# Optimization experiments

Measured on AMD Instinct MI355X. Metric: run time of the kernel, lower is better.

## Reference

```python
import jax, jax.numpy as jnp
import numpy as np

K = 8  # knn_graph(k=8, loop=True): self-loop kept, so self is among the k nearest


def knn_idx(x, k):
    # x: [N, F]. Pairwise squared distances via the expansion trick.
    x2 = jnp.sum(x * x, axis=-1)                      # [N]
    d = x2[:, None] + x2[None, :] - 2.0 * (x @ x.T)   # [N, N]
    _, idx = jax.lax.top_k(-d, k)                     # [N, k] nearest (incl. self)
    return idx


def edge_conv(x, idx, W1, b1, W2, b2):
    # PyG EdgeConv: message = nn(cat([x_i, x_j - x_i])), aggr='max'.
    # Every node has exactly k incoming edges, so scatter-max == max over the k axis.
    n, f = x.shape
    k = idx.shape[1]
    xi = x[:, None, :]                                # [N, 1, F] center
    xj = x[idx]                                       # [N, k, F] neighbors (gather)
    e = jnp.concatenate([jnp.broadcast_to(xi, (n, k, f)), xj - xi], axis=-1)  # [N,k,2F]
    h = jax.nn.relu(e @ W1 + b1) @ W2 + b2            # [N, k, out]
    return jnp.max(h, axis=1)                         # [N, out]


def setup_inputs() -> dict:
    key = jax.random.key(0)
    ks = jax.random.split(key, 9)
    B, N, F = 2, 4096, 3
    H0, H1, OUT = 64, 128, 256

    def lin(kw, fan_in, fan_out):
        bound = 1.0 / np.sqrt(fan_in)
        kw1, kw2 = jax.random.split(kw)
        W = jax.random.uniform(kw1, (fan_in, fan_out), jnp.float32, -bound, bound)
        b = jax.random.uniform(kw2, (fan_out,), jnp.float32, -bound, bound)
        return W, b

    W1, b1 = lin(ks[0], 2 * F, H0)
    W2, b2 = lin(ks[1], H0, H1)
    W3, b3 = lin(ks[2], 2 * H1, H1)
    W4, b4 = lin(ks[3], H1, OUT)
    point_cloud = jax.random.normal(ks[4], (B, N, F), jnp.float32)
    return {"point_cloud": point_cloud, "W1": W1, "b1": b1, "W2": W2, "b2": b2,
            "W3": W3, "b3": b3, "W4": W4, "b4": b4}


def reference(point_cloud, W1, b1, W2, b2, W3, b3, W4, b4):
    B, N, F = point_cloud.shape
    pts = point_cloud.reshape(B * N, F)               # knn over ALL B*N points (no batch vec)
    idx = knn_idx(jax.lax.stop_gradient(pts), K)      # [B*N, K]
    x = jax.nn.relu(edge_conv(pts, idx, W1, b1, W2, b2))
    x = edge_conv(x, idx, W3, b3, W4, b4)
    return x.reshape(B, N, -1)
```

## Files before the change

kernel.cpp:

```cpp
#include <hip/hip_runtime.h>

#define NPTS 8192
#define NSLICE 64
#define SLICE_LEN (NPTS / NSLICE)
#define KNN 8
#define SURV_CAP 48

typedef short bf16x8 __attribute__((ext_vector_type(8)));
typedef float f32x4 __attribute__((ext_vector_type(4)));

__device__ __forceinline__ unsigned short f2bf(float x) {
  unsigned int u = __float_as_uint(x);
  return (unsigned short)((u + 0x7FFF + ((u >> 16) & 1)) >> 16);
}
__device__ __forceinline__ float bf2f(unsigned short s) {
  return __uint_as_float(((unsigned int)s) << 16);
}

__device__ __forceinline__ float dist_pk(float qx, float qy, float qz,
                                         float q2, float m2x, float m2y,
                                         float m2z, float p2) {
#pragma clang fp contract(off)
  float s = __fmaf_rn(qz, m2z, __fmaf_rn(qy, m2y, __fmaf_rn(qx, m2x, p2)));
  return __fadd_rn(q2, s);
}

__device__ __forceinline__ float norm2_exact(float x, float y, float z) {
#pragma clang fp contract(off)
  return __fadd_rn(__fadd_rn(__fmul_rn(x, x), __fmul_rn(y, y)),
                   __fmul_rn(z, z));
}

__device__ __forceinline__ float med3(float a, float b, float c) {
  return __builtin_amdgcn_fmed3f(a, b, c);
}

__device__ __forceinline__ double pack_key(float d, int idx) {
  unsigned int ub = __float_as_uint(d);
  ub ^= (((unsigned int)((int)ub >> 31)) | 0x80000000u);
  unsigned int lo = (ub << 13) | (unsigned int)idx;
  unsigned int hi = 0x3ff00000u | (ub >> 19);
  return __hiloint2double((int)hi, (int)lo);
}

#define KEY_DECL                                                            \
  const double KINF = __longlong_as_double(0x7ff0000000000000LL);           \
  double k0 = KINF, k1 = KINF, k2 = KINF, k3 = KINF, k4 = KINF, k5 = KINF,  \
         k6 = KINF, k7 = KINF;
#define KB1(s)                                                              \
  {                                                                         \
    double mn = fmin(carry, k##s);                                          \
    carry = fmax(carry, k##s);                                              \
    k##s = mn;                                                              \
  }
#define KEY_INSERT(key)                                                     \
  {                                                                         \
    double carry = (key);                                                   \
    KB1(0) KB1(1) KB1(2) KB1(3) KB1(4) KB1(5) KB1(6) KB1(7)                 \
  }

#define VINS(dv)                                                            \
  {                                                                         \
    float dd = (dv);                                                        \
    v7 = med3(dd, v6, v7);                                                  \
    v6 = med3(dd, v5, v6);                                                  \
    v5 = med3(dd, v4, v5);                                                  \
    v4 = med3(dd, v3, v4);                                                  \
    v3 = med3(dd, v2, v3);                                                  \
    v2 = med3(dd, v1, v2);                                                  \
    v1 = med3(dd, v0, v1);                                                  \
    v0 = fminf(dd, v0);                                                     \
  }

#define VDECL                                                               \
  const float FINF = __uint_as_float(0x7f800000u);                          \
  float v0 = FINF, v1 = FINF, v2 = FINF, v3 = FINF, v4 = FINF, v5 = FINF,   \
        v6 = FINF, v7 = FINF;

#define VINS2(dv)                                                           \
  {                                                                         \
    float dd = (dv);                                                        \
    s1 = med3(dd, s0, s1);                                                  \
    s0 = fminf(dd, s0);                                                     \
  }

__global__ __launch_bounds__(256) void knn_vals_kernel(
    const float* __restrict__ pts, float* __restrict__ part_v,
    float4* __restrict__ pts4) {
  __shared__ float4 sp[SLICE_LEN];
  const int t = threadIdx.x;
  const int q = blockIdx.x * 256 + t;
  const int jbase = blockIdx.y * SLICE_LEN;
  for (int p = t; p < SLICE_LEN; p += 256) {
    float x = pts[(jbase + p) * 3 + 0];
    float yy = pts[(jbase + p) * 3 + 1];
    float z = pts[(jbase + p) * 3 + 2];
    float4 v = make_float4(__fmul_rn(-2.0f, x), __fmul_rn(-2.0f, yy),
                           __fmul_rn(-2.0f, z), norm2_exact(x, yy, z));
    sp[p] = v;
    if (blockIdx.x == 0) pts4[jbase + p] = v;
  }
  __syncthreads();
  const float qx = pts[q * 3 + 0], qy = pts[q * 3 + 1], qz = pts[q * 3 + 2];
  const float q2 = norm2_exact(qx, qy, qz);
  const float FINF = __uint_as_float(0x7f800000u);
  float s0 = FINF, s1 = FINF;
  for (int p = 0; p < SLICE_LEN; p += 8) {
    float4 c0 = sp[p + 0];
    float4 c1 = sp[p + 1];
    float4 c2 = sp[p + 2];
    float4 c3 = sp[p + 3];
    float4 c4 = sp[p + 4];
    float4 c5 = sp[p + 5];
    float4 c6 = sp[p + 6];
    float4 c7 = sp[p + 7];
    float d0 = dist_pk(qx, qy, qz, q2, c0.x, c0.y, c0.z, c0.w);
    float d1 = dist_pk(qx, qy, qz, q2, c1.x, c1.y, c1.z, c1.w);
    float d2 = dist_pk(qx, qy, qz, q2, c2.x, c2.y, c2.z, c2.w);
    float d3 = dist_pk(qx, qy, qz, q2, c3.x, c3.y, c3.z, c3.w);
    float d4 = dist_pk(qx, qy, qz, q2, c4.x, c4.y, c4.z, c4.w);
    float d5 = dist_pk(qx, qy, qz, q2, c5.x, c5.y, c5.z, c5.w);
    float d6 = dist_pk(qx, qy, qz, q2, c6.x, c6.y, c6.z, c6.w);
    float d7 = dist_pk(qx, qy, qz, q2, c7.x, c7.y, c7.z, c7.w);
    VINS2(d0);
    VINS2(d1);
    VINS2(d2);
    VINS2(d3);
    VINS2(d4);
    VINS2(d5);
    VINS2(d6);
    VINS2(d7);
  }
  float* o = &part_v[(size_t)(blockIdx.y * 2) * NPTS + q];
  o[0 * NPTS] = s0;
  o[1 * NPTS] = s1;
}

__global__ __launch_bounds__(256) void knn_collect_kernel(
    const float4* __restrict__ pts4, const float* __restrict__ part_v,
    int* __restrict__ nbr, const float* __restrict__ W2,
    const float* __restrict__ W3, const float* __restrict__ W4,
    unsigned short* __restrict__ W2th, unsigned short* __restrict__ W2tl,
    unsigned short* __restrict__ W3th, unsigned short* __restrict__ W3tl,
    unsigned short* __restrict__ W4ht, unsigned short* __restrict__ W4lt) {
  __shared__ double keybuf[4][SURV_CAP];
  __shared__ int scnt[4];
  __shared__ float v8s[4][8][9];
  __shared__ float smin[4][65];
  __shared__ float thrS[4];
  __shared__ unsigned long long maskS[4];
  const int t = threadIdx.x;
  if (blockIdx.x < 128) {
    const int id = blockIdx.x * 256 + t;
    const int k = id >> 8, c = id & 255;
    {
      float v = W4[k * 256 + c];
      unsigned short hi = f2bf(v);
      W4ht[c * 128 + k] = hi;
      W4lt[c * 128 + k] = f2bf(v - bf2f(hi));
    }
    {
      float v3 = (c < 128) ? W3[k * 128 + c] : W3[(128 + k) * 128 + (c - 128)];
      unsigned short h3 = f2bf(v3);
      W3th[c * 128 + k] = h3;
      W3tl[c * 128 + k] = f2bf(v3 - bf2f(h3));
    }
    if (id < NPTS) {
      const int kk = id >> 7, cc = id & 127;
      float v2 = W2[kk * 128 + cc];
      unsigned short h2 = f2bf(v2);
      W2th[cc * 64 + kk] = h2;
      W2tl[cc * 64 + kk] = f2bf(v2 - bf2f(h2));
    }
  }
  const int wv = t >> 6;
  const int lane = t & 63;
  const int q = blockIdx.x * 4 + wv;
  if (lane == 0) scnt[wv] = 0;

  if (t < 32) {
    const int lq = t >> 3, c = t & 7;
    const int qq = blockIdx.x * 4 + lq;
    VDECL;
#pragma unroll
    for (int s8 = 0; s8 < 8; ++s8) {
      const int s = c * 8 + s8;
      const float* col = &part_v[(size_t)(s * 2) * NPTS + qq];
      float a0 = col[0 * (size_t)NPTS];
      float a1 = col[1 * (size_t)NPTS];
      smin[lq][s] = a0;
      VINS(a0);
      VINS(a1);
    }
    v8s[lq][c][0] = v0;
    v8s[lq][c][1] = v1;
    v8s[lq][c][2] = v2;
    v8s[lq][c][3] = v3;
    v8s[lq][c][4] = v4;
    v8s[lq][c][5] = v5;
    v8s[lq][c][6] = v6;
    v8s[lq][c][7] = v7;
  }
  __syncthreads();

  if (t < 4) {
    const int lq = t;
    VDECL;
#pragma unroll
    for (int s = 0; s < 8; ++s) {
      VINS(v8s[lq][s][0]);
      VINS(v8s[lq][s][1]);
      VINS(v8s[lq][s][2]);
      VINS(v8s[lq][s][3]);
      VINS(v8s[lq][s][4]);
      VINS(v8s[lq][s][5]);
      VINS(v8s[lq][s][6]);
      VINS(v8s[lq][s][7]);
    }
    const float tcol = v7 + fabsf(v7) * 4e-5f + 1e-20f;
    const float tmask = v7 + fabsf(v7) * 8e-5f + 2e-20f;
    unsigned long long mk = 0;
#pragma unroll
    for (int s = 0; s < NSLICE; ++s) {
      if (smin[lq][s] <= tmask) mk |= (1ull << s);
    }
    thrS[lq] = tcol;
    maskS[lq] = mk;
  }
  __syncthreads();

  const float4 qp = pts4[q];
  const float qx = __fmul_rn(-0.5f, qp.x);
  const float qy = __fmul_rn(-0.5f, qp.y);
  const float qz = __fmul_rn(-0.5f, qp.z);
  const float q2 = qp.w;
  const float thrq = thrS[wv];
  unsigned long long m = maskS[wv];
  while (m) {
    const int s = (int)__ffsll(m) - 1;
    m &= m - 1;
    const int base = s * SLICE_LEN;
#pragma unroll
    for (int r = 0; r < SLICE_LEN / 64; ++r) {
      const int j = base + r * 64 + lane;
      const float4 cp = pts4[j];
      const float d = dist_pk(qx, qy, qz, q2, cp.x, cp.y, cp.z, cp.w);
      if (d <= thrq) {
        int slot = atomicAdd(&scnt[wv], 1);
        if (slot < SURV_CAP) keybuf[wv][slot] = pack_key(d, j);
      }
    }
  }
  __syncthreads();
  if (lane == 0) {
    int c = scnt[wv];
    if (c > SURV_CAP) c = SURV_CAP;
    KEY_DECL;
    for (int u = 0; u < c; ++u) {
      KEY_INSERT(keybuf[wv][u]);
    }
    int* o = &nbr[q * KNN];
    o[0] = __double2loint(k0) & 0x1fff;
    o[1] = __double2loint(k1) & 0x1fff;
    o[2] = __double2loint(k2) & 0x1fff;
    o[3] = __double2loint(k3) & 0x1fff;
    o[4] = __double2loint(k4) & 0x1fff;
    o[5] = __double2loint(k5) & 0x1fff;
    o[6] = __double2loint(k6) & 0x1fff;
    o[7] = __double2loint(k7) & 0x1fff;
  }
}

__global__ __launch_bounds__(256) void gemm1_fused_kernel(
    const float* __restrict__ pts, const int* __restrict__ nbr,
    const float* __restrict__ W1, const float* __restrict__ b1,
    const unsigned short* __restrict__ W2th,
    const unsigned short* __restrict__ W2tl, const float* __restrict__ b2,
    float* __restrict__ y) {
  __shared__ float es[64][6];
  __shared__ float W1s[6][64];
  __shared__ float b1s[64];
  __shared__ unsigned short H1h[64 * 72];
  __shared__ unsigned short H1l[64 * 72];
  __shared__ unsigned short Wth[64 * 72];
  __shared__ unsigned short Wtl[64 * 72];
  const int t = threadIdx.x;
  const int rowBase = blockIdx.y * 64;
  const int colBase = blockIdx.x * 64;

  for (int idx = t; idx < 384; idx += 256) W1s[idx >> 6][idx & 63] = W1[idx];
  if (t < 64) b1s[t] = b1[t];
  {
    const int colloc = t >> 2, kq = (t & 3) * 16;
    const size_t src = (size_t)(colBase + colloc) * 64 + kq;
    *(uint4*)&Wth[colloc * 72 + kq] = *(const uint4*)&W2th[src];
    *(uint4*)&Wth[colloc * 72 + kq + 8] = *(const uint4*)&W2th[src + 8];
    *(uint4*)&Wtl[colloc * 72 + kq] = *(const uint4*)&W2tl[src];
    *(uint4*)&Wtl[colloc * 72 + kq + 8] = *(const uint4*)&W2tl[src + 8];
  }
  if (t < 64) {
    int e = rowBase + t;
    int i = e >> 3;
    int j = nbr[e];
    float xi0 = pts[i * 3], xi1 = pts[i * 3 + 1], xi2 = pts[i * 3 + 2];
    es[t][0] = xi0;
    es[t][1] = xi1;
    es[t][2] = xi2;
    es[t][3] = pts[j * 3] - xi0;
    es[t][4] = pts[j * 3 + 1] - xi1;
    es[t][5] = pts[j * 3 + 2] - xi2;
  }
  __syncthreads();

  {
    const int e = t & 63, k0 = (t >> 6) * 16;
    const float f0 = es[e][0], f1 = es[e][1], f2 = es[e][2];
    const float f3 = es[e][3], f4 = es[e][4], f5 = es[e][5];
    float h[16];
#pragma unroll
    for (int k = 0; k < 16; ++k) {
      int c = k0 + k;
      float v = b1s[c];
      v = fmaf(f0, W1s[0][c], v);
      v = fmaf(f1, W1s[1][c], v);
      v = fmaf(f2, W1s[2][c], v);
      v = fmaf(f3, W1s[3][c], v);
      v = fmaf(f4, W1s[4][c], v);
      v = fmaf(f5, W1s[5][c], v);
      h[k] = fmaxf(v, 0.0f);
    }
    unsigned int hp[8], lp[8];
#pragma unroll
    for (int u = 0; u < 8; ++u) {
      unsigned short h0 = f2bf(h[2 * u]), h1 = f2bf(h[2 * u + 1]);
      hp[u] = (unsigned int)h0 | ((unsigned int)h1 << 16);
      unsigned short l0 = f2bf(h[2 * u] - bf2f(h0));
      unsigned short l1 = f2bf(h[2 * u + 1] - bf2f(h1));
      lp[u] = (unsigned int)l0 | ((unsigned int)l1 << 16);
    }
    *(uint4*)&H1h[e * 72 + k0] = make_uint4(hp[0], hp[1], hp[2], hp[3]);
    *(uint4*)&H1h[e * 72 + k0 + 8] = make_uint4(hp[4], hp[5], hp[6], hp[7]);
    *(uint4*)&H1l[e * 72 + k0] = make_uint4(lp[0], lp[1], lp[2], lp[3]);
    *(uint4*)&H1l[e * 72 + k0 + 8] = make_uint4(lp[4], lp[5], lp[6], lp[7]);
  }
  __syncthreads();

  const int lane = t & 63, w = t >> 6;
  const int qq = lane >> 4, nidx = lane & 15;
  f32x4 acc[4];
#pragma unroll
  for (int nt = 0; nt < 4; ++nt) acc[nt] = (f32x4){0.f, 0.f, 0.f, 0.f};
  bf16x8 ah0, ah1, al0, al1;
  {
    const int row = w * 16 + nidx;
    ah0 = *(const bf16x8*)&H1h[row * 72 + qq * 8];
    ah1 = *(const bf16x8*)&H1h[row * 72 + 32 + qq * 8];
    al0 = *(const bf16x8*)&H1l[row * 72 + qq * 8];
    al1 = *(const bf16x8*)&H1l[row * 72 + 32 + qq * 8];
  }
#pragma unroll
  for (int nt = 0; nt < 4; ++nt) {
    const int col = nt * 16 + nidx;
    bf16x8 bh0 = *(const bf16x8*)&Wth[col * 72 + qq * 8];
    bf16x8 bh1 = *(const bf16x8*)&Wth[col * 72 + 32 + qq * 8];
    bf16x8 bl0 = *(const bf16x8*)&Wtl[col * 72 + qq * 8];
    bf16x8 bl1 = *(const bf16x8*)&Wtl[col * 72 + 32 + qq * 8];
    acc[nt] = __builtin_amdgcn_mfma_f32_16x16x32_bf16(ah0, bh0, acc[nt], 0, 0, 0);
    acc[nt] = __builtin_amdgcn_mfma_f32_16x16x32_bf16(ah1, bh1, acc[nt], 0, 0, 0);
    acc[nt] = __builtin_amdgcn_mfma_f32_16x16x32_bf16(ah0, bl0, acc[nt], 0, 0, 0);
    acc[nt] = __builtin_amdgcn_mfma_f32_16x16x32_bf16(ah1, bl1, acc[nt], 0, 0, 0);
    acc[nt] = __builtin_amdgcn_mfma_f32_16x16x32_bf16(al0, bh0, acc[nt], 0, 0, 0);
    acc[nt] = __builtin_amdgcn_mfma_f32_16x16x32_bf16(al1, bh1, acc[nt], 0, 0, 0);
  }

  const int pt = blockIdx.y * 8 + 2 * w + (qq >> 1);
#pragma unroll
  for (int nt = 0; nt < 4; ++nt) {
    f32x4 a = acc[nt];
    float m = fmaxf(fmaxf(a[0], a[1]), fmaxf(a[2], a[3]));
    float o = fmaxf(m, __shfl_xor(m, 16, 64));
    if ((qq & 1) == 0) {
      int cg = colBase + nt * 16 + nidx;
      y[(size_t)pt * 128 + cg] = fmaxf(o + b2[cg], 0.0f);
    }
  }
}

__global__ __launch_bounds__(256) void gemm_ac_mfma_kernel(
    const float* __restrict__ y, const unsigned short* __restrict__ W3th,
    const unsigned short* __restrict__ W3tl, const float* __restrict__ bias,
    float* __restrict__ AC) {
  __shared__ unsigned short Ah[128 * 40];
  __shared__ unsigned short Al[128 * 40];
  __shared__ unsigned short Bh[128 * 40];
  __shared__ unsigned short Bl[128 * 40];
  const int t = threadIdx.x;
  const int rowBase = blockIdx.y * 128;
  const int colBase = blockIdx.x * 128;
  const int eloc = t >> 1, hh = t & 1;
  const int kb = hh * 16;
  const int lane = t & 63, w = t >> 6;
  const int q = lane >> 4, nidx = lane & 15;

  f32x4 acc[2][8];
#pragma unroll
  for (int mt = 0; mt < 2; ++mt)
#pragma unroll
    for (int nt = 0; nt < 8; ++nt) acc[mt][nt] = (f32x4){0.f, 0.f, 0.f, 0.f};

  for (int p = 0; p < 4; ++p) {
    const int k0 = p * 32;
    {
      const float* src = &y[(size_t)(rowBase + eloc) * 128 + k0 + kb];
      float h[16];
      *(float4*)&h[0] = *(const float4*)&src[0];
      *(float4*)&h[4] = *(const float4*)&src[4];
      *(float4*)&h[8] = *(const float4*)&src[8];
      *(float4*)&h[12] = *(const float4*)&src[12];
      unsigned int hp[8], lp[8];
#pragma unroll
      for (int u = 0; u < 8; ++u) {
        unsigned short h0 = f2bf(h[2 * u]), h1 = f2bf(h[2 * u + 1]);
        hp[u] = (unsigned int)h0 | ((unsigned int)h1 << 16);
        unsigned short l0 = f2bf(h[2 * u] - bf2f(h0));
        unsigned short l1 = f2bf(h[2 * u + 1] - bf2f(h1));
        lp[u] = (unsigned int)l0 | ((unsigned int)l1 << 16);
      }
      *(uint4*)&Ah[eloc * 40 + kb] = make_uint4(hp[0], hp[1], hp[2], hp[3]);
      *(uint4*)&Ah[eloc * 40 + kb + 8] = make_uint4(hp[4], hp[5], hp[6], hp[7]);
      *(uint4*)&Al[eloc * 40 + kb] = make_uint4(lp[0], lp[1], lp[2], lp[3]);
      *(uint4*)&Al[eloc * 40 + kb + 8] = make_uint4(lp[4], lp[5], lp[6], lp[7]);
    }
    {
      const size_t src = (size_t)(colBase + eloc) * 128 + k0 + kb;
      *(uint4*)&Bh[eloc * 40 + kb] = *(const uint4*)&W3th[src];
      *(uint4*)&Bh[eloc * 40 + kb + 8] = *(const uint4*)&W3th[src + 8];
      *(uint4*)&Bl[eloc * 40 + kb] = *(const uint4*)&W3tl[src];
      *(uint4*)&Bl[eloc * 40 + kb + 8] = *(const uint4*)&W3tl[src + 8];
    }
    __syncthreads();
    bf16x8 ah[2], al[2];
#pragma unroll
    for (int mt = 0; mt < 2; ++mt) {
      int row = w * 32 + mt * 16 + nidx;
      ah[mt] = *(const bf16x8*)&Ah[row * 40 + q * 8];
      al[mt] = *(const bf16x8*)&Al[row * 40 + q * 8];
    }
#pragma unroll
    for (int nt = 0; nt < 8; ++nt) {
      int col = nt * 16 + nidx;
      bf16x8 bh = *(const bf16x8*)&Bh[col * 40 + q * 8];
      bf16x8 bl = *(const bf16x8*)&Bl[col * 40 + q * 8];
#pragma unroll
      for (int mt = 0; mt < 2; ++mt) {
        acc[mt][nt] = __builtin_amdgcn_mfma_f32_16x16x32_bf16(
            ah[mt], bh, acc[mt][nt], 0, 0, 0);
        acc[mt][nt] = __builtin_amdgcn_mfma_f32_16x16x32_bf16(
            ah[mt], bl, acc[mt][nt], 0, 0, 0);
        acc[mt][nt] = __builtin_amdgcn_mfma_f32_16x16x32_bf16(
            al[mt], bh, acc[mt][nt], 0, 0, 0);
      }
    }
    __syncthreads();
  }

#pragma unroll
  for (int mt = 0; mt < 2; ++mt) {
    const int rowb = rowBase + w * 32 + mt * 16 + q * 4;
#pragma unroll
    for (int nt = 0; nt < 8; ++nt) {
      f32x4 a = acc[mt][nt];
      const int cg = colBase + nt * 16 + nidx;
      const float bb = (cg < 128) ? bias[cg] : 0.0f;
#pragma unroll
      for (int reg = 0; reg < 4; ++reg) {
        AC[(size_t)(rowb + reg) * 256 + cg] = a[reg] + bb;
      }
    }
  }
}

__global__ __launch_bounds__(256) void gemm2_mfma_kernel(
    const float* __restrict__ AC, const int* __restrict__ nbr,
    const unsigned short* __restrict__ W4ht,
    const unsigned short* __restrict__ W4lt, const float* __restrict__ b4,
    float* __restrict__ out) {
  __shared__ unsigned short H2h[128 * 40];
  __shared__ unsigned short H2l[128 * 40];
  __shared__ unsigned short Wth[128 * 40];
  __shared__ unsigned short Wtl[128 * 40];
  const int t = threadIdx.x;
  const int rowBase = blockIdx.y * 128;
  const int colBase = blockIdx.x * 128;
  const int eloc = t >> 1, hh = t & 1;
  const int kb = hh * 16;
  const int edge = rowBase + eloc;
  const int ip = edge >> 3;
  const int jp = nbr[edge];
  const float* ai_p = AC + (size_t)ip * 256;
  const float* ci_p = ai_p + 128;
  const float* cj_p = AC + (size_t)jp * 256 + 128;
  const int lane = t & 63;
  const int w = t >> 6;
  const int q = lane >> 4;
  const int nidx = lane & 15;

  f32x4 acc[2][8];
#pragma unroll
  for (int mt = 0; mt < 2; ++mt)
#pragma unroll
    for (int nt = 0; nt < 8; ++nt) acc[mt][nt] = (f32x4){0.f, 0.f, 0.f, 0.f};

  for (int p = 0; p < 4; ++p) {
    const int k0 = p * 32;
    {
      float h2[16];
      const float4* a4 = (const float4*)(ai_p + k0 + kb);
      const float4* c4 = (const float4*)(ci_p + k0 + kb);
      const float4* d4 = (const float4*)(cj_p + k0 + kb);
#pragma unroll
      for (int u = 0; u < 4; ++u) {
        float4 a = a4[u], c = c4[u], d = d4[u];
        h2[u * 4 + 0] = fmaxf(a.x + d.x - c.x, 0.f);
        h2[u * 4 + 1] = fmaxf(a.y + d.y - c.y, 0.f);
        h2[u * 4 + 2] = fmaxf(a.z + d.z - c.z, 0.f);
        h2[u * 4 + 3] = fmaxf(a.w + d.w - c.w, 0.f);
      }
      unsigned int hp[8], lp[8];
#pragma unroll
      for (int u = 0; u < 8; ++u) {
        unsigned short h0 = f2bf(h2[2 * u]), h1 = f2bf(h2[2 * u + 1]);
        hp[u] = (unsigned int)h0 | ((unsigned int)h1 << 16);
        unsigned short l0 = f2bf(h2[2 * u] - bf2f(h0));
        unsigned short l1 = f2bf(h2[2 * u + 1] - bf2f(h1));
        lp[u] = (unsigned int)l0 | ((unsigned int)l1 << 16);
      }
      *(uint4*)&H2h[eloc * 40 + kb] = make_uint4(hp[0], hp[1], hp[2], hp[3]);
      *(uint4*)&H2h[eloc * 40 + kb + 8] =
          make_uint4(hp[4], hp[5], hp[6], hp[7]);
      *(uint4*)&H2l[eloc * 40 + kb] = make_uint4(lp[0], lp[1], lp[2], lp[3]);
      *(uint4*)&H2l[eloc * 40 + kb + 8] =
          make_uint4(lp[4], lp[5], lp[6], lp[7]);
    }
    {
      const size_t src = (size_t)(colBase + eloc) * 128 + k0 + kb;
      *(uint4*)&Wth[eloc * 40 + kb] = *(const uint4*)&W4ht[src];
      *(uint4*)&Wth[eloc * 40 + kb + 8] = *(const uint4*)&W4ht[src + 8];
      *(uint4*)&Wtl[eloc * 40 + kb] = *(const uint4*)&W4lt[src];
      *(uint4*)&Wtl[eloc * 40 + kb + 8] = *(const uint4*)&W4lt[src + 8];
    }
    __syncthreads();
    bf16x8 ah[2], al[2];
#pragma unroll
    for (int mt = 0; mt < 2; ++mt) {
      int row = w * 32 + mt * 16 + nidx;
      ah[mt] = *(const bf16x8*)&H2h[row * 40 + q * 8];
      al[mt] = *(const bf16x8*)&H2l[row * 40 + q * 8];
    }
#pragma unroll
    for (int nt = 0; nt < 8; ++nt) {
      int col = nt * 16 + nidx;
      bf16x8 bh = *(const bf16x8*)&Wth[col * 40 + q * 8];
      bf16x8 bl = *(const bf16x8*)&Wtl[col * 40 + q * 8];
#pragma unroll
      for (int mt = 0; mt < 2; ++mt) {
        acc[mt][nt] = __builtin_amdgcn_mfma_f32_16x16x32_bf16(
            ah[mt], bh, acc[mt][nt], 0, 0, 0);
        acc[mt][nt] = __builtin_amdgcn_mfma_f32_16x16x32_bf16(
            ah[mt], bl, acc[mt][nt], 0, 0, 0);
        acc[mt][nt] = __builtin_amdgcn_mfma_f32_16x16x32_bf16(
            al[mt], bh, acc[mt][nt], 0, 0, 0);
      }
    }
    __syncthreads();
  }

#pragma unroll
  for (int mt = 0; mt < 2; ++mt) {
    const int ebase = rowBase + w * 32 + mt * 16;
    const int pt0 = ebase >> 3;
#pragma unroll
    for (int nt = 0; nt < 8; ++nt) {
      f32x4 a = acc[mt][nt];
      float m = fmaxf(fmaxf(a[0], a[1]), fmaxf(a[2], a[3]));
      float o = fmaxf(m, __shfl_xor(m, 16, 64));
      int cg = colBase + nt * 16 + nidx;
      if (q == 0) {
        out[(size_t)pt0 * 256 + cg] = o + b4[cg];
      } else if (q == 2) {
        out[(size_t)(pt0 + 1) * 256 + cg] = o + b4[cg];
      }
    }
  }
}

extern "C" void kernel_launch(void* const* d_in, const int* in_sizes, int n_in,
                              void* d_out, int out_size, void* d_ws,
                              size_t ws_size, hipStream_t stream) {
  const float* pts = (const float*)d_in[0];
  const float* W1 = (const float*)d_in[1];
  const float* b1 = (const float*)d_in[2];
  const float* W2 = (const float*)d_in[3];
  const float* b2 = (const float*)d_in[4];
  const float* W3 = (const float*)d_in[5];
  const float* b3 = (const float*)d_in[6];
  const float* W4 = (const float*)d_in[7];
  const float* b4 = (const float*)d_in[8];
  float* out = (float*)d_out;

  float* w = (float*)d_ws;
  float* part_v = w;
  int* nbr = (int*)(w + 4202496);
  float* y = w + 4268032;
  unsigned short* W4ht = (unsigned short*)(w + 5332992);
  unsigned short* W4lt = (unsigned short*)(w + 5349376);
  float4* pts4 = (float4*)(w + 5365760);
  unsigned short* W2th = (unsigned short*)(w + 5398528);
  unsigned short* W2tl = (unsigned short*)(w + 5402624);
  unsigned short* W3th = (unsigned short*)(w + 5406720);
  unsigned short* W3tl = (unsigned short*)(w + 5423104);
  float* AC = w;

  knn_vals_kernel<<<dim3(32, NSLICE), 256, 0, stream>>>(pts, part_v, pts4);
  knn_collect_kernel<<<2048, 256, 0, stream>>>(pts4, part_v, nbr, W2, W3, W4,
                                               W2th, W2tl, W3th, W3tl, W4ht,
                                               W4lt);

  gemm1_fused_kernel<<<dim3(2, 1024), 256, 0, stream>>>(pts, nbr, W1, b1,
                                                        W2th, W2tl, b2, y);

  gemm_ac_mfma_kernel<<<dim3(2, 64), 256, 0, stream>>>(y, W3th, W3tl, b3, AC);
  gemm2_mfma_kernel<<<dim3(2, 512), 256, 0, stream>>>(AC, nbr, W4ht, W4lt, b4,
                                                      out);
}
```

Before: 153.0 us.

## Process two queries per thread in knn and emit pre-split bf16 activations

The knn distance kernel now has each thread handle two query points (q and q+4096) against each LDS candidate. This halves the grid and reuses every shared-memory load for two distance computations. Separately, the first GEMM kernel now writes its ReLU output already split into bf16 high/low halves, so the following GEMM loads them straight into LDS instead of converting fp32 per tile. This cuts conversion work and keeps global traffic the same, at the cost of more register pressure in the knn kernel and fewer knn blocks for occupancy.

```diff
diff --git a/kernel.cpp b/kernel.cpp
--- a/kernel.cpp
+++ b/kernel.cpp
@@ -77,19 +77,13 @@
   float v0 = FINF, v1 = FINF, v2 = FINF, v3 = FINF, v4 = FINF, v5 = FINF,   \
         v6 = FINF, v7 = FINF;
 
-#define VINS2(dv)                                                           \
-  {                                                                         \
-    float dd = (dv);                                                        \
-    s1 = med3(dd, s0, s1);                                                  \
-    s0 = fminf(dd, s0);                                                     \
-  }
-
 __global__ __launch_bounds__(256) void knn_vals_kernel(
     const float* __restrict__ pts, float* __restrict__ part_v,
     float4* __restrict__ pts4) {
   __shared__ float4 sp[SLICE_LEN];
   const int t = threadIdx.x;
-  const int q = blockIdx.x * 256 + t;
+  const int qa = blockIdx.x * 256 + t;
+  const int qb = qa + 4096;
   const int jbase = blockIdx.y * SLICE_LEN;
   for (int p = t; p < SLICE_LEN; p += 256) {
     float x = pts[(jbase + p) * 3 + 0];
@@ -101,39 +95,54 @@
     if (blockIdx.x == 0) pts4[jbase + p] = v;
   }
   __syncthreads();
-  const float qx = pts[q * 3 + 0], qy = pts[q * 3 + 1], qz = pts[q * 3 + 2];
-  const float q2 = norm2_exact(qx, qy, qz);
+  const float ax = pts[qa * 3 + 0], ay = pts[qa * 3 + 1], az = pts[qa * 3 + 2];
+  const float a2 = norm2_exact(ax, ay, az);
+  const float bx = pts[qb * 3 + 0], by = pts[qb * 3 + 1], bz = pts[qb * 3 + 2];
+  const float b2 = norm2_exact(bx, by, bz);
   const float FINF = __uint_as_float(0x7f800000u);
-  float s0 = FINF, s1 = FINF;
-  for (int p = 0; p < SLICE_LEN; p += 8) {
+  float sa0 = FINF, sa1 = FINF, sb0 = FINF, sb1 = FINF;
+#define V2A(dv)                                                             \
+  {                                                                         \
+    float dd = (dv);                                                        \
+    sa1 = med3(dd, sa0, sa1);                                               \
+    sa0 = fminf(dd, sa0);                                                   \
+  }
+#define V2B(dv)                                                             \
+  {                                                                         \
+    float dd = (dv);                                                        \
+    sb1 = med3(dd, sb0, sb1);                                               \
+    sb0 = fminf(dd, sb0);                                                   \
+  }
+  for (int p = 0; p < SLICE_LEN; p += 4) {
     float4 c0 = sp[p + 0];
     float4 c1 = sp[p + 1];
     float4 c2 = sp[p + 2];
     float4 c3 = sp[p + 3];
-    float4 c4 = sp[p + 4];
-    float4 c5 = sp[p + 5];
-    float4 c6 = sp[p + 6];
-    float4 c7 = sp[p + 7];
-    float d0 = dist_pk(qx, qy, qz, q2, c0.x, c0.y, c0.z, c0.w);
-    float d1 = dist_pk(qx, qy, qz, q2, c1.x, c1.y, c1.z, c1.w);
-    float d2 = dist_pk(qx, qy, qz, q2, c2.x, c2.y, c2.z, c2.w);
-    float d3 = dist_pk(qx, qy, qz, q2, c3.x, c3.y, c3.z, c3.w);
-    float d4 = dist_pk(qx, qy, qz, q2, c4.x, c4.y, c4.z, c4.w);
-    float d5 = dist_pk(qx, qy, qz, q2, c5.x, c5.y, c5.z, c5.w);
-    float d6 = dist_pk(qx, qy, qz, q2, c6.x, c6.y, c6.z, c6.w);
-    float d7 = dist_pk(qx, qy, qz, q2, c7.x, c7.y, c7.z, c7.w);
-    VINS2(d0);
-    VINS2(d1);
-    VINS2(d2);
-    VINS2(d3);
-    VINS2(d4);
-    VINS2(d5);
-    VINS2(d6);
-    VINS2(d7);
-  }
-  float* o = &part_v[(size_t)(blockIdx.y * 2) * NPTS + q];
-  o[0 * NPTS] = s0;
-  o[1 * NPTS] = s1;
+    float da0 = dist_pk(ax, ay, az, a2, c0.x, c0.y, c0.z, c0.w);
+    float db0 = dist_pk(bx, by, bz, b2, c0.x, c0.y, c0.z, c0.w);
+    float da1 = dist_pk(ax, ay, az, a2, c1.x, c1.y, c1.z, c1.w);
+    float db1 = dist_pk(bx, by, bz, b2, c1.x, c1.y, c1.z, c1.w);
+    float da2 = dist_pk(ax, ay, az, a2, c2.x, c2.y, c2.z, c2.w);
+    float db2 = dist_pk(bx, by, bz, b2, c2.x, c2.y, c2.z, c2.w);
+    float da3 = dist_pk(ax, ay, az, a2, c3.x, c3.y, c3.z, c3.w);
+    float db3 = dist_pk(bx, by, bz, b2, c3.x, c3.y, c3.z, c3.w);
+    V2A(da0);
+    V2B(db0);
+    V2A(da1);
+    V2B(db1);
+    V2A(da2);
+    V2B(db2);
+    V2A(da3);
+    V2B(db3);
+  }
+#undef V2A
+#undef V2B
+  float* oa = &part_v[(size_t)(blockIdx.y * 2) * NPTS + qa];
+  oa[0 * NPTS] = sa0;
+  oa[1 * NPTS] = sa1;
+  float* ob = &part_v[(size_t)(blockIdx.y * 2) * NPTS + qb];
+  ob[0 * NPTS] = sb0;
+  ob[1 * NPTS] = sb1;
 }
 
 __global__ __launch_bounds__(256) void knn_collect_kernel(
@@ -276,7 +285,7 @@
     const float* __restrict__ W1, const float* __restrict__ b1,
     const unsigned short* __restrict__ W2th,
     const unsigned short* __restrict__ W2tl, const float* __restrict__ b2,
-    float* __restrict__ y) {
+    unsigned short* __restrict__ yh, unsigned short* __restrict__ yl) {
   __shared__ float es[64][6];
   __shared__ float W1s[6][64];
   __shared__ float b1s[64];
@@ -381,13 +390,17 @@
     float o = fmaxf(m, __shfl_xor(m, 16, 64));
     if ((qq & 1) == 0) {
       int cg = colBase + nt * 16 + nidx;
-      y[(size_t)pt * 128 + cg] = fmaxf(o + b2[cg], 0.0f);
+      float v = fmaxf(o + b2[cg], 0.0f);
+      unsigned short hi = f2bf(v);
+      yh[(size_t)pt * 128 + cg] = hi;
+      yl[(size_t)pt * 128 + cg] = f2bf(v - bf2f(hi));
     }
   }
 }
 
 __global__ __launch_bounds__(256) void gemm_ac_mfma_kernel(
-    const float* __restrict__ y, const unsigned short* __restrict__ W3th,
+    const unsigned short* __restrict__ yh, const unsigned short* __restrict__ yl,
+    const unsigned short* __restrict__ W3th,
     const unsigned short* __restrict__ W3tl, const float* __restrict__ bias,
     float* __restrict__ AC) {
   __shared__ unsigned short Ah[128 * 40];
@@ -411,25 +424,11 @@
   for (int p = 0; p < 4; ++p) {
     const int k0 = p * 32;
     {
-      const float* src = &y[(size_t)(rowBase + eloc) * 128 + k0 + kb];
-      float h[16];
-      *(float4*)&h[0] = *(const float4*)&src[0];
-      *(float4*)&h[4] = *(const float4*)&src[4];
-      *(float4*)&h[8] = *(const float4*)&src[8];
-      *(float4*)&h[12] = *(const float4*)&src[12];
-      unsigned int hp[8], lp[8];
-#pragma unroll
-      for (int u = 0; u < 8; ++u) {
-        unsigned short h0 = f2bf(h[2 * u]), h1 = f2bf(h[2 * u + 1]);
-        hp[u] = (unsigned int)h0 | ((unsigned int)h1 << 16);
-        unsigned short l0 = f2bf(h[2 * u] - bf2f(h0));
-        unsigned short l1 = f2bf(h[2 * u + 1] - bf2f(h1));
-        lp[u] = (unsigned int)l0 | ((unsigned int)l1 << 16);
-      }
-      *(uint4*)&Ah[eloc * 40 + kb] = make_uint4(hp[0], hp[1], hp[2], hp[3]);
-      *(uint4*)&Ah[eloc * 40 + kb + 8] = make_uint4(hp[4], hp[5], hp[6], hp[7]);
-      *(uint4*)&Al[eloc * 40 + kb] = make_uint4(lp[0], lp[1], lp[2], lp[3]);
-      *(uint4*)&Al[eloc * 40 + kb + 8] = make_uint4(lp[4], lp[5], lp[6], lp[7]);
+      const size_t src = (size_t)(rowBase + eloc) * 128 + k0 + kb;
+      *(uint4*)&Ah[eloc * 40 + kb] = *(const uint4*)&yh[src];
+      *(uint4*)&Ah[eloc * 40 + kb + 8] = *(const uint4*)&yh[src + 8];
+      *(uint4*)&Al[eloc * 40 + kb] = *(const uint4*)&yl[src];
+      *(uint4*)&Al[eloc * 40 + kb + 8] = *(const uint4*)&yl[src + 8];
     }
     {
       const size_t src = (size_t)(colBase + eloc) * 128 + k0 + kb;
@@ -611,7 +610,8 @@
   float* w = (float*)d_ws;
   float* part_v = w;
   int* nbr = (int*)(w + 4202496);
-  float* y = w + 4268032;
+  unsigned short* yh = (unsigned short*)(w + 4268032);
+  unsigned short* yl = (unsigned short*)(w + 4792320);
   unsigned short* W4ht = (unsigned short*)(w + 5332992);
   unsigned short* W4lt = (unsigned short*)(w + 5349376);
   float4* pts4 = (float4*)(w + 5365760);
@@ -621,15 +621,17 @@
   unsigned short* W3tl = (unsigned short*)(w + 5423104);
   float* AC = w;
 
-  knn_vals_kernel<<<dim3(32, NSLICE), 256, 0, stream>>>(pts, part_v, pts4);
+  knn_vals_kernel<<<dim3(16, NSLICE), 256, 0, stream>>>(pts, part_v, pts4);
   knn_collect_kernel<<<2048, 256, 0, stream>>>(pts4, part_v, nbr, W2, W3, W4,
                                                W2th, W2tl, W3th, W3tl, W4ht,
                                                W4lt);
 
   gemm1_fused_kernel<<<dim3(2, 1024), 256, 0, stream>>>(pts, nbr, W1, b1,
-                                                        W2th, W2tl, b2, y);
-
-  gemm_ac_mfma_kernel<<<dim3(2, 64), 256, 0, stream>>>(y, W3th, W3tl, b3, AC);
+                                                        W2th, W2tl, b2, yh,
+                                                        yl);
+
+  gemm_ac_mfma_kernel<<<dim3(2, 64), 256, 0, stream>>>(yh, yl, W3th, W3tl,
+                                                       b3, AC);
   gemm2_mfma_kernel<<<dim3(2, 512), 256, 0, stream>>>(AC, nbr, W4ht, W4lt, b4,
                                                       out);
 }
```

Result: no change. 153.3 us (+0.2%).
